# Kernel optimization log

Measured on AMD Instinct MI355X. Metric: run time of the kernel, lower is better.

Reference implementation:

```python
import jax, jax.numpy as jnp
import numpy as np

BETA = 0.95
THR = 0.8
SLOPE = 25.0  # fast_sigmoid surrogate slope


@jax.custom_vjp
def spike(x):
    # Heaviside forward, fast-sigmoid surrogate backward (snntorch surrogate.fast_sigmoid)
    return (x > 0).astype(x.dtype)

def _spike_fwd(x):
    return spike(x), x

def _spike_bwd(x, g):
    return (g / (SLOPE * jnp.abs(x) + 1.0) ** 2,)

spike.defvjp(_spike_fwd, _spike_bwd)


def setup_inputs() -> dict:
    key = jax.random.key(0)
    k1, k2, k3 = jax.random.split(key, 3)
    B, T, D, H, C = 512, 2000, 20, 128, 10
    x = jax.random.normal(k1, (B, T, D), dtype=jnp.float32)
    # kaiming_normal_ with nonlinearity='linear': std = 1/sqrt(fan_in)
    W1 = jax.random.normal(k2, (H, D), dtype=jnp.float32) / np.sqrt(D)
    b1 = jnp.zeros((H,), jnp.float32)
    W2 = jax.random.normal(k3, (C, H), dtype=jnp.float32) / np.sqrt(H)
    b2 = jnp.zeros((C,), jnp.float32)
    return {"x": x, "W1": W1, "b1": b1, "W2": W2, "b2": b2}


def reference(x, W1, b1, W2, b2):
    B, T, D = x.shape
    H = W1.shape[0]

    def step(mem, xt):
        cur = xt @ W1.T + b1                                  # [B,H]
        # snntorch Leaky: reset based on PREVIOUS mem (detached), subtract mechanism
        reset = jax.lax.stop_gradient(spike(mem - THR))
        mem_new = BETA * mem + cur - reset * THR
        spk = spike(mem_new - THR)
        return mem_new, spk

    mem0 = jnp.zeros((B, H), x.dtype)
    _, spks = jax.lax.scan(step, mem0, jnp.swapaxes(x, 0, 1))  # spks: [T,B,H]

    spikeCounts = spks.sum(0)                                  # [B,H]
    # sum_t fc2(spk_t) = spikeCounts @ W2^T + T * b2
    logits = (spikeCounts @ W2.T + T * b2) / T
    logits = logits + 0.1 * ((spikeCounts / (T + 1e-6)) @ W2.T + b2)
    return logits
```

## Files before the change

kernel.cpp:

```cpp
#include <hip/hip_runtime.h>
#include <stdint.h>

#define Bdim 512
#define Tdim 2000
#define Ddim 20
#define Hdim 128
#define Cdim 10
#define TT   64
#define NCH  32
#define BETA 0.95f
#define THR  0.8f

typedef float f32x2 __attribute__((ext_vector_type(2)));
typedef float f32x4 __attribute__((ext_vector_type(4)));
typedef int   i32x4 __attribute__((ext_vector_type(4)));

#define CVT_HILO(HI, LO, F0, F1) {                                                     \
    asm volatile("v_cvt_pk_bf16_f32 %0, %1, %2" : "=v"(HI) : "v"(F0), "v"(F1));        \
    const float h0f_ = __uint_as_float((HI) << 16);                                    \
    const float h1f_ = __uint_as_float((HI) & 0xFFFF0000u);                            \
    const float l0_ = (F0) - h0f_;  const float l1_ = (F1) - h1f_;                     \
    asm volatile("v_cvt_pk_bf16_f32 %0, %1, %2" : "=v"(LO) : "v"(l0_), "v"(l1_)); }

#define MFMA0(ACC, A8, B8) \
  asm volatile("v_mfma_f32_16x16x32_bf16 %0, %1, %2, 0"  : "=v"(ACC) : "v"(A8), "v"(B8));
#define MFMA(ACC, A8, B8)  \
  asm volatile("v_mfma_f32_16x16x32_bf16 %0, %1, %2, %0" : "+v"(ACC) : "v"(A8), "v"(B8));

__global__ __launch_bounds__(256, 1) void snn_spec4_kernel(
    const float* __restrict__ x,
    const float* __restrict__ W1,
    const float* __restrict__ b1,
    const float* __restrict__ W2,
    const float* __restrict__ b2,
    float* __restrict__ out)
{
  const int b   = blockIdx.x;
  const int tid = threadIdx.x;
  const int wid = tid >> 6;
  const int l   = tid & 63;
  const int r   = l & 15;
  const int g   = l >> 4;

  const bool flip = ((b >> 8) & 1) != 0;
  const bool isP  = flip ? (wid >= 2) : (wid < 2);
  const int  pwid = wid & 1;
  const int  swid = wid & 1;

  __shared__ __align__(16) float xraw[2][TT * Ddim];
  __shared__ __align__(16) float cur[2][TT * 132];
  __shared__ float cnt_s[Hdim];

  const float* xb = x + (size_t)b * (Tdim * Ddim);
  const float* const clampMax = x + (size_t)Bdim * Tdim * Ddim - 4;

  const uint32_t xrawB = (uint32_t)(uintptr_t)&xraw[0][0];
  const uint32_t curB  = (uint32_t)(uintptr_t)&cur[0][0];

  i32x4 bhi[8], blo[8];
  f32x4 zero4, ovr;
  bool  sel23 = false, g3f = false;
  if (isP) {
    const bool g2 = (g == 2);
    g3f   = (g == 3);
    sel23 = g2 | g3f;
    zero4[0]=0.f; zero4[1]=0.f; zero4[2]=0.f; zero4[3]=0.f;
    ovr = zero4; if (g2) ovr[0] = 1.0f;
#pragma unroll
    for (int ni = 0; ni < 8; ++ni) {
      const int hh = ni * 16 + r;
      float wv[8];
#pragma unroll
      for (int j = 0; j < 8; ++j) {
        const int k = 8 * g + j;
        wv[j] = (k < Ddim) ? W1[hh * Ddim + k] : ((k == Ddim) ? b1[hh] : 0.0f);
      }
#pragma unroll
      for (int d = 0; d < 4; ++d) {
        const uint32_t u0 = __float_as_uint(wv[2*d]), u1 = __float_as_uint(wv[2*d+1]);
        const uint32_t h0 = (u0 + 0x8000u) & 0xFFFF0000u;
        const uint32_t h1 = (u1 + 0x8000u) & 0xFFFF0000u;
        bhi[ni][d] = (int)(h1 | (h0 >> 16));
        const float l0 = wv[2*d]   - __uint_as_float(h0);
        const float l1 = wv[2*d+1] - __uint_as_float(h1);
        const uint32_t e0 = (__float_as_uint(l0) + 0x8000u) & 0xFFFF0000u;
        const uint32_t e1 = (__float_as_uint(l1) + 0x8000u) & 0xFFFF0000u;
        blo[ni][d] = (int)(e1 | (e0 >> 16));
      }
    }
  }

  float    mem = 0.0f;
  bool     sp  = false;
  uint32_t cnt = 0u;
  f32x2    negT2; negT2[0] = -THR; negT2[1] = -THR;

#define STAGE(CH, BUF) do {                                                            \
    const float* g0_ = xb + (CH) * 1280 + pwid * 640 + l * 4;                          \
    char* lb_ = (char*)&xraw[0][0] + (BUF) * 5120 + pwid * 2560 + l * 16;              \
    const float* p0_ = g0_;        if (p0_ > clampMax) p0_ = clampMax;                 \
    const float* p1_ = g0_ + 256;  if (p1_ > clampMax) p1_ = clampMax;                 \
    __builtin_amdgcn_global_load_lds(                                                  \
      (const __attribute__((address_space(1))) unsigned int*)p0_,                      \
      (__attribute__((address_space(3))) unsigned int*)lb_, 16, 0, 0);                 \
    __builtin_amdgcn_global_load_lds(                                                  \
      (const __attribute__((address_space(1))) unsigned int*)p1_,                      \
      (__attribute__((address_space(3))) unsigned int*)(lb_ + 1024), 16, 0, 0);        \
    if (l < 32) {                                                                      \
      const float* p2_ = g0_ + 512;  if (p2_ > clampMax) p2_ = clampMax;               \
      __builtin_amdgcn_global_load_lds(                                                \
        (const __attribute__((address_space(1))) unsigned int*)p2_,                    \
        (__attribute__((address_space(3))) unsigned int*)(lb_ + 2048), 16, 0, 0);      \
    } } while (0)

#define VM0()  asm volatile("s_waitcnt vmcnt(0)" ::: "memory");
#define LGW(N) asm volatile("s_waitcnt lgkmcnt(" #N ")" ::: "memory"); __builtin_amdgcn_sched_barrier(0);
#define BAR()  __builtin_amdgcn_sched_barrier(0); __builtin_amdgcn_s_barrier(); __builtin_amdgcn_sched_barrier(0);

#define CW2(NI, AC)                                                                    \
    asm volatile("ds_write2_b32 %0, %1, %2 offset0:%c3 offset1:%c4"                    \
                 :: "v"(cwb_),  "v"(AC[0]), "v"(AC[1]), "n"(16*(NI)), "n"(16*(NI)+132)); \
    asm volatile("ds_write2_b32 %0, %1, %2 offset0:%c3 offset1:%c4"                    \
                 :: "v"(cwb2_), "v"(AC[2]), "v"(AC[3]), "n"(16*(NI)), "n"(16*(NI)+132));

#define CWRM(MTIDX, P0,P1,P2,P3,P4,P5,P6,P7) {                                         \
    const uint32_t cwb_  = curB + (uint32_t)(pbuf * 33792 + 528 * ((MTIDX) * 16 + 4 * g) + 4 * r); \
    const uint32_t cwb2_ = cwb_ + 1056u;                                               \
    CW2(0,P0) CW2(1,P1) CW2(2,P2) CW2(3,P3) CW2(4,P4) CW2(5,P5) CW2(6,P6) CW2(7,P7) }

#define SELA(A0, A1) { A0 = g3f ? zero4 : A0;  A1 = sel23 ? ovr : A1; }

#define CVT8(AHI, ALO, A0, A1) {                                                       \
    uint32_t h_, lo_;                                                                  \
    CVT_HILO(h_, lo_, A0[0], A0[1]) AHI[0]=(int)h_; ALO[0]=(int)lo_;                   \
    CVT_HILO(h_, lo_, A0[2], A0[3]) AHI[1]=(int)h_; ALO[1]=(int)lo_;                   \
    CVT_HILO(h_, lo_, A1[0], A1[1]) AHI[2]=(int)h_; ALO[2]=(int)lo_;                   \
    CVT_HILO(h_, lo_, A1[2], A1[3]) AHI[3]=(int)h_; ALO[3]=(int)lo_; }

#define MM24(AHI, ALO, C0,C1,C2,C3,C4,C5,C6,C7)                                        \
    MFMA0(C0, ALO, bhi[0]) MFMA0(C1, ALO, bhi[1]) MFMA0(C2, ALO, bhi[2])               \
    MFMA0(C3, ALO, bhi[3]) MFMA0(C4, ALO, bhi[4]) MFMA0(C5, ALO, bhi[5])               \
    MFMA0(C6, ALO, bhi[6]) MFMA0(C7, ALO, bhi[7])                                      \
    MFMA (C0, AHI, blo[0]) MFMA (C1, AHI, blo[1]) MFMA (C2, AHI, blo[2])               \
    MFMA (C3, AHI, blo[3]) MFMA (C4, AHI, blo[4]) MFMA (C5, AHI, blo[5])               \
    MFMA (C6, AHI, blo[6]) MFMA (C7, AHI, blo[7])                                      \
    MFMA (C0, AHI, bhi[0]) MFMA (C1, AHI, bhi[1]) MFMA (C2, AHI, bhi[2])               \
    MFMA (C3, AHI, bhi[3]) MFMA (C4, AHI, bhi[4]) MFMA (C5, AHI, bhi[5])               \
    MFMA (C6, AHI, bhi[6]) MFMA (C7, AHI, bhi[7])

#define GEMM2() {                                                                      \
    const uint32_t afb_ = xrawB + (uint32_t)(pbuf * 5120 + (2*pwid) * 1280 + 80 * r + 32 * g); \
    f32x4 a00_, a01_, a10_, a11_;                                                      \
    asm volatile("ds_read_b128 %0, %1 offset:0"    : "=v"(a00_) : "v"(afb_));          \
    asm volatile("ds_read_b128 %0, %1 offset:16"   : "=v"(a01_) : "v"(afb_));          \
    asm volatile("ds_read_b128 %0, %1 offset:1280" : "=v"(a10_) : "v"(afb_));          \
    asm volatile("ds_read_b128 %0, %1 offset:1296" : "=v"(a11_) : "v"(afb_));          \
    LGW(2)                                                                             \
    SELA(a00_, a01_)                                                                   \
    i32x4 ahi0_, alo0_;  CVT8(ahi0_, alo0_, a00_, a01_)                                \
    asm volatile("s_nop 2");                                                           \
    f32x4 c00,c01,c02,c03,c04,c05,c06,c07;                                             \
    MM24(ahi0_, alo0_, c00,c01,c02,c03,c04,c05,c06,c07)                                \
    LGW(0)                                                                             \
    SELA(a10_, a11_)                                                                   \
    i32x4 ahi1_, alo1_;  CVT8(ahi1_, alo1_, a10_, a11_)                                \
    asm volatile("s_nop 2");                                                           \
    f32x4 c10,c11,c12,c13,c14,c15,c16,c17;                                             \
    MM24(ahi1_, alo1_, c10,c11,c12,c13,c14,c15,c16,c17)                                \
    asm volatile("s_nop 7"); asm volatile("s_nop 4");                                  \
    CWRM(2*pwid,     c00,c01,c02,c03,c04,c05,c06,c07)                                  \
    CWRM(2*pwid + 1, c10,c11,c12,c13,c14,c15,c16,c17) }

#define GEMM_TAIL() {                                                                  \
    const uint32_t afb_ = xrawB + (uint32_t)(pbuf * 5120 + 80 * r + 32 * g);           \
    f32x4 a00_, a01_;                                                                  \
    asm volatile("ds_read_b128 %0, %1 offset:0"  : "=v"(a00_) : "v"(afb_));            \
    asm volatile("ds_read_b128 %0, %1 offset:16" : "=v"(a01_) : "v"(afb_));            \
    LGW(0)                                                                             \
    SELA(a00_, a01_)                                                                   \
    i32x4 ahi0_, alo0_;  CVT8(ahi0_, alo0_, a00_, a01_)                                \
    asm volatile("s_nop 2");                                                           \
    f32x4 c00,c01,c02,c03,c04,c05,c06,c07;                                             \
    MM24(ahi0_, alo0_, c00,c01,c02,c03,c04,c05,c06,c07)                                \
    asm volatile("s_nop 7"); asm volatile("s_nop 4");                                  \
    CWRM(0, c00,c01,c02,c03,c04,c05,c06,c07) }

#define RD2A(PR, AD) asm volatile("ds_read2_b32 %0, %1 offset0:0 offset1:132" : "=v"(PR) : "v"(AD));
#define CONSUME(PR) {                                                                  \
    f32x2 cm_; asm("v_pk_add_f32 %0, %1, %2" : "=v"(cm_) : "v"(PR), "v"(negT2));       \
    float mP_ = fmaf(BETA, mem, PR[0]);                                                \
    float mM_ = fmaf(BETA, mem, cm_[0]);                                               \
    mem = sp ? mM_ : mP_;                                                              \
    sp  = mem > THR;                                                                   \
    cnt += sp ? 1u : 0u;                                                               \
    mP_ = fmaf(BETA, mem, PR[1]);                                                      \
    mM_ = fmaf(BETA, mem, cm_[1]);                                                     \
    mem = sp ? mM_ : mP_;                                                              \
    sp  = mem > THR;                                                                   \
    cnt += sp ? 1u : 0u; }

#define SFI(RGA, RGB, SA, SB) { LGW(6) CONSUME(pr##RGA) CONSUME(pr##RGB)               \
    { const uint32_t adA_ = spB + (uint32_t)((SA) * 1056); RD2A(pr##RGA, adA_) }       \
    { const uint32_t adB_ = spB + (uint32_t)((SB) * 1056); RD2A(pr##RGB, adB_) } }
#define SFT(RGA, RGB, W) { LGW(W) CONSUME(pr##RGA) CONSUME(pr##RGB) }

#define SCAN_PRE()                                                                     \
    f32x2 pr0, pr1, pr2, pr3, pr4, pr5, pr6, pr7;                                      \
    RD2A(pr0, spB)          RD2A(pr1, spB + 1056u)  RD2A(pr2, spB + 2112u)             \
    RD2A(pr3, spB + 3168u)  RD2A(pr4, spB + 4224u)  RD2A(pr5, spB + 5280u)             \
    RD2A(pr6, spB + 6336u)  RD2A(pr7, spB + 7392u)

#define SCAN_FULL() {                                                                  \
    SCAN_PRE()                                                                         \
    SFI(0,1,  8, 9) SFI(2,3, 10,11) SFI(4,5, 12,13) SFI(6,7, 14,15)                    \
    SFI(0,1, 16,17) SFI(2,3, 18,19) SFI(4,5, 20,21) SFI(6,7, 22,23)                    \
    SFI(0,1, 24,25) SFI(2,3, 26,27) SFI(4,5, 28,29) SFI(6,7, 30,31)                    \
    SFT(0,1,6) SFT(2,3,4) SFT(4,5,2) SFT(6,7,0) }

#define SCAN_TAIL() {                                                                  \
    SCAN_PRE()                                                                         \
    SFT(0,1,6) SFT(2,3,4) SFT(4,5,2) SFT(6,7,0) }

  const uint32_t spB0 = curB + (uint32_t)((swid * 64 + l) * 4);

  if (isP) STAGE(0, 0);

#pragma unroll 1
  for (int ph = 0; ph <= NCH; ++ph) {
    if (isP) {
      if (ph <= NCH - 1) {
        VM0()
        if (ph < NCH - 1) STAGE(ph + 1, (ph + 1) & 1);
        const uint32_t pbuf = (uint32_t)(ph & 1);
        if (ph < NCH - 1) {
          GEMM2()
        } else if (pwid == 0) {
          GEMM_TAIL()
        }
        LGW(0)
      }
    } else {
      if (ph >= 1) {
        const uint32_t spB = spB0 + (uint32_t)(((ph - 1) & 1) * 33792);
        if (ph - 1 < NCH - 1) { SCAN_FULL() }
        else                  { SCAN_TAIL() }
        if (ph == NCH) cnt_s[swid * 64 + l] = (float)cnt;
      }
    }
    BAR()
  }

  __syncthreads();

  if (tid < Cdim) {
    float dot = 0.0f;
#pragma unroll
    for (int k = 0; k < Hdim; ++k)
      dot = fmaf(cnt_s[k], W2[tid * Hdim + k], dot);
    const float Tf = (float)Tdim;
    const float scale = 1.0f / Tf + 0.1f / (Tf + 1e-6f);
    out[b * Cdim + tid] = fmaf(dot, scale, 1.1f * b2[tid]);
  }
}

extern "C" void kernel_launch(void* const* d_in, const int* in_sizes, int n_in,
                              void* d_out, int out_size, void* d_ws, size_t ws_size,
                              hipStream_t stream) {
  const float* x  = (const float*)d_in[0];
  const float* W1 = (const float*)d_in[1];
  const float* b1 = (const float*)d_in[2];
  const float* W2 = (const float*)d_in[3];
  const float* b2 = (const float*)d_in[4];
  float* out = (float*)d_out;

  snn_spec4_kernel<<<dim3(Bdim), dim3(256), 0, stream>>>(x, W1, b1, W2, b2, out);
}
```

Measured before the change: 58.73 us.

## Split hidden dimension across two blocks per batch row with atomic output reduction

Each batch row is now handled by two blocks, each owning half of the hidden units (64). The time chunk is halved to 32 steps so the GEMM and scan loops keep their shapes. Partial logits are combined with atomicAdd into an output zeroed by a memset beforehand. The aim is to double the grid to fill more CUs and shorten each block's serial scan work. The cost is that x is loaded twice, there are twice as many barrier phases, and an extra memset launch plus atomics are added.

```diff
diff --git a/kernel.cpp b/kernel.cpp
--- a/kernel.cpp
+++ b/kernel.cpp
@@ -6,8 +6,8 @@
 #define Ddim 20
 #define Hdim 128
 #define Cdim 10
-#define TT   64
-#define NCH  32
+#define TT   32
+#define NCHF 62
 #define BETA 0.95f
 #define THR  0.8f
 
@@ -27,7 +27,7 @@
 #define MFMA(ACC, A8, B8)  \
   asm volatile("v_mfma_f32_16x16x32_bf16 %0, %1, %2, %0" : "+v"(ACC) : "v"(A8), "v"(B8));
 
-__global__ __launch_bounds__(256, 1) void snn_spec4_kernel(
+__global__ __launch_bounds__(256, 1) void snn_spec5_kernel(
     const float* __restrict__ x,
     const float* __restrict__ W1,
     const float* __restrict__ b1,
@@ -35,29 +35,31 @@
     const float* __restrict__ b2,
     float* __restrict__ out)
 {
-  const int b   = blockIdx.x;
+  const int blk = blockIdx.x;
+  const int bb  = blk >> 1;
+  const int hh  = blk & 1;
   const int tid = threadIdx.x;
   const int wid = tid >> 6;
   const int l   = tid & 63;
   const int r   = l & 15;
   const int g   = l >> 4;
 
-  const bool flip = ((b >> 8) & 1) != 0;
+  const bool flip = ((blk >> 8) & 1) != 0;
   const bool isP  = flip ? (wid >= 2) : (wid < 2);
   const int  pwid = wid & 1;
   const int  swid = wid & 1;
 
   __shared__ __align__(16) float xraw[2][TT * Ddim];
-  __shared__ __align__(16) float cur[2][TT * 132];
-  __shared__ float cnt_s[Hdim];
-
-  const float* xb = x + (size_t)b * (Tdim * Ddim);
+  __shared__ __align__(16) float cur[2][TT * 66];
+  __shared__ float cnt_s[64];
+
+  const float* xb = x + (size_t)bb * (Tdim * Ddim);
   const float* const clampMax = x + (size_t)Bdim * Tdim * Ddim - 4;
 
   const uint32_t xrawB = (uint32_t)(uintptr_t)&xraw[0][0];
   const uint32_t curB  = (uint32_t)(uintptr_t)&cur[0][0];
 
-  i32x4 bhi[8], blo[8];
+  i32x4 bhi[4], blo[4];
   f32x4 zero4, ovr;
   bool  sel23 = false, g3f = false;
   if (isP) {
@@ -67,13 +69,13 @@
     zero4[0]=0.f; zero4[1]=0.f; zero4[2]=0.f; zero4[3]=0.f;
     ovr = zero4; if (g2) ovr[0] = 1.0f;
 #pragma unroll
-    for (int ni = 0; ni < 8; ++ni) {
-      const int hh = ni * 16 + r;
+    for (int ni = 0; ni < 4; ++ni) {
+      const int hhh = hh * 64 + ni * 16 + r;
       float wv[8];
 #pragma unroll
       for (int j = 0; j < 8; ++j) {
         const int k = 8 * g + j;
-        wv[j] = (k < Ddim) ? W1[hh * Ddim + k] : ((k == Ddim) ? b1[hh] : 0.0f);
+        wv[j] = (k < Ddim) ? W1[hhh * Ddim + k] : ((k == Ddim) ? b1[hhh] : 0.0f);
       }
 #pragma unroll
       for (int d = 0; d < 4; ++d) {
@@ -96,40 +98,24 @@
   f32x2    negT2; negT2[0] = -THR; negT2[1] = -THR;
 
 #define STAGE(CH, BUF) do {                                                            \
-    const float* g0_ = xb + (CH) * 1280 + pwid * 640 + l * 4;                          \
-    char* lb_ = (char*)&xraw[0][0] + (BUF) * 5120 + pwid * 2560 + l * 16;              \
-    const float* p0_ = g0_;        if (p0_ > clampMax) p0_ = clampMax;                 \
-    const float* p1_ = g0_ + 256;  if (p1_ > clampMax) p1_ = clampMax;                 \
+    const float* g0_ = xb + (CH) * 640 + pwid * 320 + l * 4;                           \
+    char* lb_ = (char*)&xraw[0][0] + (BUF) * 2560 + pwid * 1280 + l * 16;              \
+    const float* p0_ = g0_;  if (p0_ > clampMax) p0_ = clampMax;                       \
     __builtin_amdgcn_global_load_lds(                                                  \
       (const __attribute__((address_space(1))) unsigned int*)p0_,                      \
       (__attribute__((address_space(3))) unsigned int*)lb_, 16, 0, 0);                 \
-    __builtin_amdgcn_global_load_lds(                                                  \
-      (const __attribute__((address_space(1))) unsigned int*)p1_,                      \
-      (__attribute__((address_space(3))) unsigned int*)(lb_ + 1024), 16, 0, 0);        \
-    if (l < 32) {                                                                      \
-      const float* p2_ = g0_ + 512;  if (p2_ > clampMax) p2_ = clampMax;               \
+    if (l < 16) {                                                                      \
+      const float* p1_ = g0_ + 256;  if (p1_ > clampMax) p1_ = clampMax;               \
       __builtin_amdgcn_global_load_lds(                                                \
-        (const __attribute__((address_space(1))) unsigned int*)p2_,                    \
-        (__attribute__((address_space(3))) unsigned int*)(lb_ + 2048), 16, 0, 0);      \
+        (const __attribute__((address_space(1))) unsigned int*)p1_,                    \
+        (__attribute__((address_space(3))) unsigned int*)(lb_ + 1024), 16, 0, 0);      \
     } } while (0)
 
 #define VM0()  asm volatile("s_waitcnt vmcnt(0)" ::: "memory");
 #define LGW(N) asm volatile("s_waitcnt lgkmcnt(" #N ")" ::: "memory"); __builtin_amdgcn_sched_barrier(0);
 #define BAR()  __builtin_amdgcn_sched_barrier(0); __builtin_amdgcn_s_barrier(); __builtin_amdgcn_sched_barrier(0);
 
-#define CW2(NI, AC)                                                                    \
-    asm volatile("ds_write2_b32 %0, %1, %2 offset0:%c3 offset1:%c4"                    \
-                 :: "v"(cwb_),  "v"(AC[0]), "v"(AC[1]), "n"(16*(NI)), "n"(16*(NI)+132)); \
-    asm volatile("ds_write2_b32 %0, %1, %2 offset0:%c3 offset1:%c4"                    \
-                 :: "v"(cwb2_), "v"(AC[2]), "v"(AC[3]), "n"(16*(NI)), "n"(16*(NI)+132));
-
-#define CWRM(MTIDX, P0,P1,P2,P3,P4,P5,P6,P7) {                                         \
-    const uint32_t cwb_  = curB + (uint32_t)(pbuf * 33792 + 528 * ((MTIDX) * 16 + 4 * g) + 4 * r); \
-    const uint32_t cwb2_ = cwb_ + 1056u;                                               \
-    CW2(0,P0) CW2(1,P1) CW2(2,P2) CW2(3,P3) CW2(4,P4) CW2(5,P5) CW2(6,P6) CW2(7,P7) }
-
 #define SELA(A0, A1) { A0 = g3f ? zero4 : A0;  A1 = sel23 ? ovr : A1; }
-
 #define CVT8(AHI, ALO, A0, A1) {                                                       \
     uint32_t h_, lo_;                                                                  \
     CVT_HILO(h_, lo_, A0[0], A0[1]) AHI[0]=(int)h_; ALO[0]=(int)lo_;                   \
@@ -137,55 +123,37 @@
     CVT_HILO(h_, lo_, A1[0], A1[1]) AHI[2]=(int)h_; ALO[2]=(int)lo_;                   \
     CVT_HILO(h_, lo_, A1[2], A1[3]) AHI[3]=(int)h_; ALO[3]=(int)lo_; }
 
-#define MM24(AHI, ALO, C0,C1,C2,C3,C4,C5,C6,C7)                                        \
-    MFMA0(C0, ALO, bhi[0]) MFMA0(C1, ALO, bhi[1]) MFMA0(C2, ALO, bhi[2])               \
-    MFMA0(C3, ALO, bhi[3]) MFMA0(C4, ALO, bhi[4]) MFMA0(C5, ALO, bhi[5])               \
-    MFMA0(C6, ALO, bhi[6]) MFMA0(C7, ALO, bhi[7])                                      \
-    MFMA (C0, AHI, blo[0]) MFMA (C1, AHI, blo[1]) MFMA (C2, AHI, blo[2])               \
-    MFMA (C3, AHI, blo[3]) MFMA (C4, AHI, blo[4]) MFMA (C5, AHI, blo[5])               \
-    MFMA (C6, AHI, blo[6]) MFMA (C7, AHI, blo[7])                                      \
-    MFMA (C0, AHI, bhi[0]) MFMA (C1, AHI, bhi[1]) MFMA (C2, AHI, bhi[2])               \
-    MFMA (C3, AHI, bhi[3]) MFMA (C4, AHI, bhi[4]) MFMA (C5, AHI, bhi[5])               \
-    MFMA (C6, AHI, bhi[6]) MFMA (C7, AHI, bhi[7])
-
-#define GEMM2() {                                                                      \
-    const uint32_t afb_ = xrawB + (uint32_t)(pbuf * 5120 + (2*pwid) * 1280 + 80 * r + 32 * g); \
-    f32x4 a00_, a01_, a10_, a11_;                                                      \
-    asm volatile("ds_read_b128 %0, %1 offset:0"    : "=v"(a00_) : "v"(afb_));          \
-    asm volatile("ds_read_b128 %0, %1 offset:16"   : "=v"(a01_) : "v"(afb_));          \
-    asm volatile("ds_read_b128 %0, %1 offset:1280" : "=v"(a10_) : "v"(afb_));          \
-    asm volatile("ds_read_b128 %0, %1 offset:1296" : "=v"(a11_) : "v"(afb_));          \
-    LGW(2)                                                                             \
-    SELA(a00_, a01_)                                                                   \
-    i32x4 ahi0_, alo0_;  CVT8(ahi0_, alo0_, a00_, a01_)                                \
+#define MM12(AHI, ALO, C0,C1,C2,C3)                                                    \
+    MFMA0(C0, ALO, bhi[0]) MFMA0(C1, ALO, bhi[1])                                      \
+    MFMA0(C2, ALO, bhi[2]) MFMA0(C3, ALO, bhi[3])                                      \
+    MFMA (C0, AHI, blo[0]) MFMA (C1, AHI, blo[1])                                      \
+    MFMA (C2, AHI, blo[2]) MFMA (C3, AHI, blo[3])                                      \
+    MFMA (C0, AHI, bhi[0]) MFMA (C1, AHI, bhi[1])                                      \
+    MFMA (C2, AHI, bhi[2]) MFMA (C3, AHI, bhi[3])
+
+#define CW2(NI, AC)                                                                    \
+    asm volatile("ds_write2_b32 %0, %1, %2 offset0:%c3 offset1:%c4"                    \
+                 :: "v"(cwb_),  "v"(AC[0]), "v"(AC[1]), "n"(16*(NI)), "n"(16*(NI)+66)); \
+    asm volatile("ds_write2_b32 %0, %1, %2 offset0:%c3 offset1:%c4"                    \
+                 :: "v"(cwb2_), "v"(AC[2]), "v"(AC[3]), "n"(16*(NI)), "n"(16*(NI)+66));
+
+#define GEMM1(TLOC) {                                                                  \
+    const uint32_t afb_ = xrawB + (uint32_t)(pbuf * 2560 + (TLOC) * 80 + 80 * r + 32 * g); \
+    f32x4 a0_, a1_;                                                                    \
+    asm volatile("ds_read_b128 %0, %1 offset:0"  : "=v"(a0_) : "v"(afb_));             \
+    asm volatile("ds_read_b128 %0, %1 offset:16" : "=v"(a1_) : "v"(afb_));             \
+    LGW(0)                                                                             \
+    SELA(a0_, a1_)                                                                     \
+    i32x4 ahi_, alo_;  CVT8(ahi_, alo_, a0_, a1_)                                      \
     asm volatile("s_nop 2");                                                           \
-    f32x4 c00,c01,c02,c03,c04,c05,c06,c07;                                             \
-    MM24(ahi0_, alo0_, c00,c01,c02,c03,c04,c05,c06,c07)                                \
-    LGW(0)                                                                             \
-    SELA(a10_, a11_)                                                                   \
-    i32x4 ahi1_, alo1_;  CVT8(ahi1_, alo1_, a10_, a11_)                                \
-    asm volatile("s_nop 2");                                                           \
-    f32x4 c10,c11,c12,c13,c14,c15,c16,c17;                                             \
-    MM24(ahi1_, alo1_, c10,c11,c12,c13,c14,c15,c16,c17)                                \
+    f32x4 c0_, c1_, c2_, c3_;                                                          \
+    MM12(ahi_, alo_, c0_, c1_, c2_, c3_)                                               \
     asm volatile("s_nop 7"); asm volatile("s_nop 4");                                  \
-    CWRM(2*pwid,     c00,c01,c02,c03,c04,c05,c06,c07)                                  \
-    CWRM(2*pwid + 1, c10,c11,c12,c13,c14,c15,c16,c17) }
-
-#define GEMM_TAIL() {                                                                  \
-    const uint32_t afb_ = xrawB + (uint32_t)(pbuf * 5120 + 80 * r + 32 * g);           \
-    f32x4 a00_, a01_;                                                                  \
-    asm volatile("ds_read_b128 %0, %1 offset:0"  : "=v"(a00_) : "v"(afb_));            \
-    asm volatile("ds_read_b128 %0, %1 offset:16" : "=v"(a01_) : "v"(afb_));            \
-    LGW(0)                                                                             \
-    SELA(a00_, a01_)                                                                   \
-    i32x4 ahi0_, alo0_;  CVT8(ahi0_, alo0_, a00_, a01_)                                \
-    asm volatile("s_nop 2");                                                           \
-    f32x4 c00,c01,c02,c03,c04,c05,c06,c07;                                             \
-    MM24(ahi0_, alo0_, c00,c01,c02,c03,c04,c05,c06,c07)                                \
-    asm volatile("s_nop 7"); asm volatile("s_nop 4");                                  \
-    CWRM(0, c00,c01,c02,c03,c04,c05,c06,c07) }
-
-#define RD2A(PR, AD) asm volatile("ds_read2_b32 %0, %1 offset0:0 offset1:132" : "=v"(PR) : "v"(AD));
+    const uint32_t cwb_  = curB + (uint32_t)(pbuf * 8448 + 264 * ((TLOC) + 4 * g) + 4 * r); \
+    const uint32_t cwb2_ = cwb_ + 528u;                                                \
+    CW2(0, c0_) CW2(1, c1_) CW2(2, c2_) CW2(3, c3_) }
+
+#define RD2A(PR, AD) asm volatile("ds_read2_b32 %0, %1 offset0:0 offset1:66" : "=v"(PR) : "v"(AD));
 #define CONSUME(PR) {                                                                  \
     f32x2 cm_; asm("v_pk_add_f32 %0, %1, %2" : "=v"(cm_) : "v"(PR), "v"(negT2));       \
     float mP_ = fmaf(BETA, mem, PR[0]);                                                \
@@ -200,66 +168,65 @@
     cnt += sp ? 1u : 0u; }
 
 #define SFI(RGA, RGB, SA, SB) { LGW(6) CONSUME(pr##RGA) CONSUME(pr##RGB)               \
-    { const uint32_t adA_ = spB + (uint32_t)((SA) * 1056); RD2A(pr##RGA, adA_) }       \
-    { const uint32_t adB_ = spB + (uint32_t)((SB) * 1056); RD2A(pr##RGB, adB_) } }
+    { const uint32_t adA_ = spB + (uint32_t)((SA) * 528); RD2A(pr##RGA, adA_) }        \
+    { const uint32_t adB_ = spB + (uint32_t)((SB) * 528); RD2A(pr##RGB, adB_) } }
 #define SFT(RGA, RGB, W) { LGW(W) CONSUME(pr##RGA) CONSUME(pr##RGB) }
 
 #define SCAN_PRE()                                                                     \
     f32x2 pr0, pr1, pr2, pr3, pr4, pr5, pr6, pr7;                                      \
-    RD2A(pr0, spB)          RD2A(pr1, spB + 1056u)  RD2A(pr2, spB + 2112u)             \
-    RD2A(pr3, spB + 3168u)  RD2A(pr4, spB + 4224u)  RD2A(pr5, spB + 5280u)             \
-    RD2A(pr6, spB + 6336u)  RD2A(pr7, spB + 7392u)
-
-#define SCAN_FULL() {                                                                  \
+    RD2A(pr0, spB)          RD2A(pr1, spB + 528u)   RD2A(pr2, spB + 1056u)             \
+    RD2A(pr3, spB + 1584u)  RD2A(pr4, spB + 2112u)  RD2A(pr5, spB + 2640u)             \
+    RD2A(pr6, spB + 3168u)  RD2A(pr7, spB + 3696u)
+
+#define SCAN_FULL() {                                             \
     SCAN_PRE()                                                                         \
     SFI(0,1,  8, 9) SFI(2,3, 10,11) SFI(4,5, 12,13) SFI(6,7, 14,15)                    \
-    SFI(0,1, 16,17) SFI(2,3, 18,19) SFI(4,5, 20,21) SFI(6,7, 22,23)                    \
-    SFI(0,1, 24,25) SFI(2,3, 26,27) SFI(4,5, 28,29) SFI(6,7, 30,31)                    \
     SFT(0,1,6) SFT(2,3,4) SFT(4,5,2) SFT(6,7,0) }
 
-#define SCAN_TAIL() {                                                                  \
+#define SCAN_TAIL() {                                              \
     SCAN_PRE()                                                                         \
     SFT(0,1,6) SFT(2,3,4) SFT(4,5,2) SFT(6,7,0) }
 
-  const uint32_t spB0 = curB + (uint32_t)((swid * 64 + l) * 4);
+  const uint32_t spB0 = curB + (uint32_t)((swid * 32 + (l & 31)) * 4);
 
   if (isP) STAGE(0, 0);
 
 #pragma unroll 1
-  for (int ph = 0; ph <= NCH; ++ph) {
+  for (int ph = 0; ph <= NCHF + 1; ++ph) {
     if (isP) {
-      if (ph <= NCH - 1) {
+      if (ph <= NCHF) {
         VM0()
-        if (ph < NCH - 1) STAGE(ph + 1, (ph + 1) & 1);
+        if (ph < NCHF) STAGE(ph + 1, (ph + 1) & 1);
         const uint32_t pbuf = (uint32_t)(ph & 1);
-        if (ph < NCH - 1) {
-          GEMM2()
+        if (ph < NCHF) {
+          GEMM1(pwid * 16)
         } else if (pwid == 0) {
-          GEMM_TAIL()
+          GEMM1(0)
         }
         LGW(0)
       }
     } else {
       if (ph >= 1) {
-        const uint32_t spB = spB0 + (uint32_t)(((ph - 1) & 1) * 33792);
-        if (ph - 1 < NCH - 1) { SCAN_FULL() }
-        else                  { SCAN_TAIL() }
-        if (ph == NCH) cnt_s[swid * 64 + l] = (float)cnt;
+        const uint32_t spB = spB0 + (uint32_t)(((ph - 1) & 1) * 8448);
+        if (ph - 1 < NCHF) { SCAN_FULL() }
+        else               { SCAN_TAIL() }
       }
     }
     BAR()
   }
 
+  if (!isP && l < 32) cnt_s[swid * 32 + (l & 31)] = (float)cnt;
   __syncthreads();
 
   if (tid < Cdim) {
     float dot = 0.0f;
 #pragma unroll
-    for (int k = 0; k < Hdim; ++k)
-      dot = fmaf(cnt_s[k], W2[tid * Hdim + k], dot);
+    for (int k = 0; k < 64; ++k)
+      dot = fmaf(cnt_s[k], W2[tid * Hdim + hh * 64 + k], dot);
     const float Tf = (float)Tdim;
     const float scale = 1.0f / Tf + 0.1f / (Tf + 1e-6f);
-    out[b * Cdim + tid] = fmaf(dot, scale, 1.1f * b2[tid]);
+    float val = dot * scale + (hh == 0 ? 1.1f * b2[tid] : 0.0f);
+    atomicAdd(&out[bb * Cdim + tid], val);
   }
 }
 
@@ -273,5 +240,6 @@
   const float* b2 = (const float*)d_in[4];
   float* out = (float*)d_out;
 
-  snn_spec4_kernel<<<dim3(Bdim), dim3(256), 0, stream>>>(x, W1, b1, W2, b2, out);
+  hipMemsetAsync(out, 0, (size_t)Bdim * Cdim * sizeof(float), stream);
+  snn_spec5_kernel<<<dim3(Bdim * 2), dim3(256), 0, stream>>>(x, W1, b1, W2, b2, out);
 }
```

New measurement: 98.24 us. +67.3%, slower.

## Transpose cur staging buffer to hidden-major layout with 128-bit LDS writes/reads

Applied to the files above, without the earlier changes.

Changes the shared-memory cur buffer from time-major [T][132] to hidden-major [H][66] so each scan lane reads four consecutive timesteps with one ds_read_b128. The GEMM waves now store MFMA accumulator quads with ds_write_b128 instead of paired ds_write2_b32. This cuts the number of LDS instructions on both the producer and the consumer side of the serial scan. The padding of 66 floats per row is meant to avoid bank conflicts, but the wider accesses may still conflict.

```diff
diff --git a/kernel.cpp b/kernel.cpp
--- a/kernel.cpp
+++ b/kernel.cpp
@@ -27,7 +27,7 @@
 #define MFMA(ACC, A8, B8)  \
   asm volatile("v_mfma_f32_16x16x32_bf16 %0, %1, %2, %0" : "+v"(ACC) : "v"(A8), "v"(B8));
 
-__global__ __launch_bounds__(256, 1) void snn_spec4_kernel(
+__global__ __launch_bounds__(256, 1) void snn_spec6_kernel(
     const float* __restrict__ x,
     const float* __restrict__ W1,
     const float* __restrict__ b1,
@@ -48,7 +48,7 @@
   const int  swid = wid & 1;
 
   __shared__ __align__(16) float xraw[2][TT * Ddim];
-  __shared__ __align__(16) float cur[2][TT * 132];
+  __shared__ __align__(16) float cur[2][Hdim * 66];
   __shared__ float cnt_s[Hdim];
 
   const float* xb = x + (size_t)b * (Tdim * Ddim);
@@ -117,17 +117,6 @@
 #define LGW(N) asm volatile("s_waitcnt lgkmcnt(" #N ")" ::: "memory"); __builtin_amdgcn_sched_barrier(0);
 #define BAR()  __builtin_amdgcn_sched_barrier(0); __builtin_amdgcn_s_barrier(); __builtin_amdgcn_sched_barrier(0);
 
-#define CW2(NI, AC)                                                                    \
-    asm volatile("ds_write2_b32 %0, %1, %2 offset0:%c3 offset1:%c4"                    \
-                 :: "v"(cwb_),  "v"(AC[0]), "v"(AC[1]), "n"(16*(NI)), "n"(16*(NI)+132)); \
-    asm volatile("ds_write2_b32 %0, %1, %2 offset0:%c3 offset1:%c4"                    \
-                 :: "v"(cwb2_), "v"(AC[2]), "v"(AC[3]), "n"(16*(NI)), "n"(16*(NI)+132));
-
-#define CWRM(MTIDX, P0,P1,P2,P3,P4,P5,P6,P7) {                                         \
-    const uint32_t cwb_  = curB + (uint32_t)(pbuf * 33792 + 528 * ((MTIDX) * 16 + 4 * g) + 4 * r); \
-    const uint32_t cwb2_ = cwb_ + 1056u;                                               \
-    CW2(0,P0) CW2(1,P1) CW2(2,P2) CW2(3,P3) CW2(4,P4) CW2(5,P5) CW2(6,P6) CW2(7,P7) }
-
 #define SELA(A0, A1) { A0 = g3f ? zero4 : A0;  A1 = sel23 ? ovr : A1; }
 
 #define CVT8(AHI, ALO, A0, A1) {                                                       \
@@ -147,6 +136,12 @@
     MFMA (C0, AHI, bhi[0]) MFMA (C1, AHI, bhi[1]) MFMA (C2, AHI, bhi[2])               \
     MFMA (C3, AHI, bhi[3]) MFMA (C4, AHI, bhi[4]) MFMA (C5, AHI, bhi[5])               \
     MFMA (C6, AHI, bhi[6]) MFMA (C7, AHI, bhi[7])
+
+#define WQ(CWB, AC, NI) \
+    asm volatile("ds_write_b128 %0, %1 offset:%c2" :: "v"(CWB), "v"(AC), "n"(4224*(NI)));
+#define WTILE8(CWB, P0,P1,P2,P3,P4,P5,P6,P7)                                           \
+    WQ(CWB,P0,0) WQ(CWB,P1,1) WQ(CWB,P2,2) WQ(CWB,P3,3)                                \
+    WQ(CWB,P4,4) WQ(CWB,P5,5) WQ(CWB,P6,6) WQ(CWB,P7,7)
 
 #define GEMM2() {                                                                      \
     const uint32_t afb_ = xrawB + (uint32_t)(pbuf * 5120 + (2*pwid) * 1280 + 80 * r + 32 * g); \
@@ -168,8 +163,9 @@
     f32x4 c10,c11,c12,c13,c14,c15,c16,c17;                                             \
     MM24(ahi1_, alo1_, c10,c11,c12,c13,c14,c15,c16,c17)                                \
     asm volatile("s_nop 7"); asm volatile("s_nop 4");                                  \
-    CWRM(2*pwid,     c00,c01,c02,c03,c04,c05,c06,c07)                                  \
-    CWRM(2*pwid + 1, c10,c11,c12,c13,c14,c15,c16,c17) }
+    const uint32_t cwA_ = curB + (uint32_t)(pbuf * 33792 + 264 * r + 128 * pwid + 16 * g); \
+    WTILE8(cwA_,       c00,c01,c02,c03,c04,c05,c06,c07)                                \
+    WTILE8(cwA_ + 64u, c10,c11,c12,c13,c14,c15,c16,c17) }
 
 #define GEMM_TAIL() {                                                                  \
     const uint32_t afb_ = xrawB + (uint32_t)(pbuf * 5120 + 80 * r + 32 * g);           \
@@ -183,45 +179,73 @@
     f32x4 c00,c01,c02,c03,c04,c05,c06,c07;                                             \
     MM24(ahi0_, alo0_, c00,c01,c02,c03,c04,c05,c06,c07)                                \
     asm volatile("s_nop 7"); asm volatile("s_nop 4");                                  \
-    CWRM(0, c00,c01,c02,c03,c04,c05,c06,c07) }
-
-#define RD2A(PR, AD) asm volatile("ds_read2_b32 %0, %1 offset0:0 offset1:132" : "=v"(PR) : "v"(AD));
-#define CONSUME(PR) {                                                                  \
-    f32x2 cm_; asm("v_pk_add_f32 %0, %1, %2" : "=v"(cm_) : "v"(PR), "v"(negT2));       \
-    float mP_ = fmaf(BETA, mem, PR[0]);                                                \
-    float mM_ = fmaf(BETA, mem, cm_[0]);                                               \
+    const uint32_t cwT_ = curB + (uint32_t)(pbuf * 33792 + 264 * r + 16 * g);          \
+    WTILE8(cwT_, c00,c01,c02,c03,c04,c05,c06,c07) }
+
+#define RDQ(Q, AD, OFF) \
+    asm volatile("ds_read_b128 %0, %1 offset:%c2" : "=v"(Q) : "v"(AD), "n"(OFF));
+
+#define CONSUME2(C0V, C1V) {                                                           \
+    float mP_ = fmaf(BETA, mem, C0V);                                                  \
+    float mM_ = fmaf(BETA, mem, C0V - THR);                                            \
     mem = sp ? mM_ : mP_;                                                              \
     sp  = mem > THR;                                                                   \
     cnt += sp ? 1u : 0u;                                                               \
-    mP_ = fmaf(BETA, mem, PR[1]);                                                      \
-    mM_ = fmaf(BETA, mem, cm_[1]);                                                     \
+    mP_ = fmaf(BETA, mem, C1V);                                                        \
+    mM_ = fmaf(BETA, mem, C1V - THR);                                                  \
     mem = sp ? mM_ : mP_;                                                              \
     sp  = mem > THR;                                                                   \
     cnt += sp ? 1u : 0u; }
 
-#define SFI(RGA, RGB, SA, SB) { LGW(6) CONSUME(pr##RGA) CONSUME(pr##RGB)               \
-    { const uint32_t adA_ = spB + (uint32_t)((SA) * 1056); RD2A(pr##RGA, adA_) }       \
-    { const uint32_t adB_ = spB + (uint32_t)((SB) * 1056); RD2A(pr##RGB, adB_) } }
-#define SFT(RGA, RGB, W) { LGW(W) CONSUME(pr##RGA) CONSUME(pr##RGB) }
-
-#define SCAN_PRE()                                                                     \
-    f32x2 pr0, pr1, pr2, pr3, pr4, pr5, pr6, pr7;                                      \
-    RD2A(pr0, spB)          RD2A(pr1, spB + 1056u)  RD2A(pr2, spB + 2112u)             \
-    RD2A(pr3, spB + 3168u)  RD2A(pr4, spB + 4224u)  RD2A(pr5, spB + 5280u)             \
-    RD2A(pr6, spB + 6336u)  RD2A(pr7, spB + 7392u)
-
-#define SCAN_FULL() {                                                                  \
-    SCAN_PRE()                                                                         \
-    SFI(0,1,  8, 9) SFI(2,3, 10,11) SFI(4,5, 12,13) SFI(6,7, 14,15)                    \
-    SFI(0,1, 16,17) SFI(2,3, 18,19) SFI(4,5, 20,21) SFI(6,7, 22,23)                    \
-    SFI(0,1, 24,25) SFI(2,3, 26,27) SFI(4,5, 28,29) SFI(6,7, 30,31)                    \
-    SFT(0,1,6) SFT(2,3,4) SFT(4,5,2) SFT(6,7,0) }
-
-#define SCAN_TAIL() {                                                                  \
-    SCAN_PRE()                                                                         \
-    SFT(0,1,6) SFT(2,3,4) SFT(4,5,2) SFT(6,7,0) }
-
-  const uint32_t spB0 = curB + (uint32_t)((swid * 64 + l) * 4);
+#define CONSUME4(Q) {                                                                  \
+    f32x2 p01_; p01_[0] = Q[0]; p01_[1] = Q[1];                                        \
+    f32x2 p23_; p23_[0] = Q[2]; p23_[1] = Q[3];                                        \
+    f32x2 cm01_, cm23_;                                                                \
+    asm("v_pk_add_f32 %0, %1, %2" : "=v"(cm01_) : "v"(p01_), "v"(negT2));              \
+    asm("v_pk_add_f32 %0, %1, %2" : "=v"(cm23_) : "v"(p23_), "v"(negT2));              \
+    { float mP_ = fmaf(BETA, mem, Q[0]);                                               \
+      float mM_ = fmaf(BETA, mem, cm01_[0]);                                           \
+      mem = sp ? mM_ : mP_;  sp = mem > THR;  cnt += sp ? 1u : 0u;                     \
+      mP_ = fmaf(BETA, mem, Q[1]);                                                     \
+      mM_ = fmaf(BETA, mem, cm01_[1]);                                                 \
+      mem = sp ? mM_ : mP_;  sp = mem > THR;  cnt += sp ? 1u : 0u;                     \
+      mP_ = fmaf(BETA, mem, Q[2]);                                                     \
+      mM_ = fmaf(BETA, mem, cm23_[0]);                                                 \
+      mem = sp ? mM_ : mP_;  sp = mem > THR;  cnt += sp ? 1u : 0u;                     \
+      mP_ = fmaf(BETA, mem, Q[3]);                                                     \
+      mM_ = fmaf(BETA, mem, cm23_[1]);                                                 \
+      mem = sp ? mM_ : mP_;  sp = mem > THR;  cnt += sp ? 1u : 0u; } }
+
+#define SCAN_FULL(SPB) {                                                               \
+    f32x4 q0,q1,q2,q3,q4,q5;                                                           \
+    RDQ(q0,SPB,0)  RDQ(q1,SPB,16) RDQ(q2,SPB,32)                                       \
+    RDQ(q3,SPB,48) RDQ(q4,SPB,64) RDQ(q5,SPB,80)                                       \
+    LGW(5) CONSUME4(q0) RDQ(q0,SPB,96)                                                 \
+    LGW(5) CONSUME4(q1) RDQ(q1,SPB,112)                                                \
+    LGW(5) CONSUME4(q2) RDQ(q2,SPB,128)                                                \
+    LGW(5) CONSUME4(q3) RDQ(q3,SPB,144)                                                \
+    LGW(5) CONSUME4(q4) RDQ(q4,SPB,160)                                                \
+    LGW(5) CONSUME4(q5) RDQ(q5,SPB,176)                                                \
+    LGW(5) CONSUME4(q0) RDQ(q0,SPB,192)                                                \
+    LGW(5) CONSUME4(q1) RDQ(q1,SPB,208)                                                \
+    LGW(5) CONSUME4(q2) RDQ(q2,SPB,224)                                                \
+    LGW(5) CONSUME4(q3) RDQ(q3,SPB,240)                                                \
+    LGW(5) CONSUME4(q4)                                                                \
+    LGW(4) CONSUME4(q5)                                                                \
+    LGW(3) CONSUME4(q0)                                                                \
+    LGW(2) CONSUME4(q1)                                                                \
+    LGW(1) CONSUME4(q2)                                                                \
+    LGW(0) CONSUME4(q3) }
+
+#define SCAN_TAIL(SPB) {                                                               \
+    f32x4 q0,q1,q2,q3;                                                                 \
+    RDQ(q0,SPB,0) RDQ(q1,SPB,16) RDQ(q2,SPB,32) RDQ(q3,SPB,48)                         \
+    LGW(3) CONSUME4(q0)                                                                \
+    LGW(2) CONSUME4(q1)                                                                \
+    LGW(1) CONSUME4(q2)                                                                \
+    LGW(0) CONSUME4(q3) }
+
+  const uint32_t spB0 = curB + (uint32_t)((swid * 64 + l) * 264);
 
   if (isP) STAGE(0, 0);
 
@@ -242,8 +266,8 @@
     } else {
       if (ph >= 1) {
         const uint32_t spB = spB0 + (uint32_t)(((ph - 1) & 1) * 33792);
-        if (ph - 1 < NCH - 1) { SCAN_FULL() }
-        else                  { SCAN_TAIL() }
+        if (ph - 1 < NCH - 1) { SCAN_FULL(spB) }
+        else                  { SCAN_TAIL(spB) }
         if (ph == NCH) cnt_s[swid * 64 + l] = (float)cnt;
       }
     }
@@ -273,5 +297,5 @@
   const float* b2 = (const float*)d_in[4];
   float* out = (float*)d_out;
 
-  snn_spec4_kernel<<<dim3(Bdim), dim3(256), 0, stream>>>(x, W1, b1, W2, b2, out);
+  snn_spec6_kernel<<<dim3(Bdim), dim3(256), 0, stream>>>(x, W1, b1, W2, b2, out);
 }
```

Result: slower. 122.9 us (+109.3%).

## Double waves per block: four GEMM producer and four scan consumer waves

Applied to the files above, without the earlier changes.

Block size grows from 256 to 512 threads. Each producer wave now handles one 16-row time tile instead of two, and each scan wave covers 32 hidden units instead of 64, with the upper 32 lanes duplicating the work. Staging loads are split over four waves, and the per-block flip of the producer/consumer role assignment is removed. The goal is to shorten the per-chunk critical path of both the GEMM and the serial scan, at the cost of more waves per block, redundant scan lanes and more barrier participants.

```diff
diff --git a/kernel.cpp b/kernel.cpp
--- a/kernel.cpp
+++ b/kernel.cpp
@@ -27,7 +27,7 @@
 #define MFMA(ACC, A8, B8)  \
   asm volatile("v_mfma_f32_16x16x32_bf16 %0, %1, %2, %0" : "+v"(ACC) : "v"(A8), "v"(B8));
 
-__global__ __launch_bounds__(256, 1) void snn_spec4_kernel(
+__global__ __launch_bounds__(512, 1) void snn_spec8_kernel(
     const float* __restrict__ x,
     const float* __restrict__ W1,
     const float* __restrict__ b1,
@@ -42,10 +42,9 @@
   const int r   = l & 15;
   const int g   = l >> 4;
 
-  const bool flip = ((b >> 8) & 1) != 0;
-  const bool isP  = flip ? (wid >= 2) : (wid < 2);
-  const int  pwid = wid & 1;
-  const int  swid = wid & 1;
+  const bool isP  = (wid < 4);
+  const int  pwid = wid & 3;
+  const int  swid = wid & 3;
 
   __shared__ __align__(16) float xraw[2][TT * Ddim];
   __shared__ __align__(16) float cur[2][TT * 132];
@@ -96,21 +95,17 @@
   f32x2    negT2; negT2[0] = -THR; negT2[1] = -THR;
 
 #define STAGE(CH, BUF) do {                                                            \
-    const float* g0_ = xb + (CH) * 1280 + pwid * 640 + l * 4;                          \
-    char* lb_ = (char*)&xraw[0][0] + (BUF) * 5120 + pwid * 2560 + l * 16;              \
-    const float* p0_ = g0_;        if (p0_ > clampMax) p0_ = clampMax;                 \
-    const float* p1_ = g0_ + 256;  if (p1_ > clampMax) p1_ = clampMax;                 \
+    const float* g0_ = xb + (CH) * 1280 + pwid * 320 + l * 4;                          \
+    char* lb_ = (char*)&xraw[0][0] + (BUF) * 5120 + pwid * 1280 + l * 16;              \
+    const float* p0_ = g0_;  if (p0_ > clampMax) p0_ = clampMax;                       \
     __builtin_amdgcn_global_load_lds(                                                  \
       (const __attribute__((address_space(1))) unsigned int*)p0_,                      \
       (__attribute__((address_space(3))) unsigned int*)lb_, 16, 0, 0);                 \
-    __builtin_amdgcn_global_load_lds(                                                  \
-      (const __attribute__((address_space(1))) unsigned int*)p1_,                      \
-      (__attribute__((address_space(3))) unsigned int*)(lb_ + 1024), 16, 0, 0);        \
-    if (l < 32) {                                                                      \
-      const float* p2_ = g0_ + 512;  if (p2_ > clampMax) p2_ = clampMax;               \
+    if (l < 16) {                                                                      \
+      const float* p1_ = g0_ + 256;  if (p1_ > clampMax) p1_ = clampMax;               \
       __builtin_amdgcn_global_load_lds(                                                \
-        (const __attribute__((address_space(1))) unsigned int*)p2_,                    \
-        (__attribute__((address_space(3))) unsigned int*)(lb_ + 2048), 16, 0, 0);      \
+        (const __attribute__((address_space(1))) unsigned int*)p1_,                    \
+        (__attribute__((address_space(3))) unsigned int*)(lb_ + 1024), 16, 0, 0);      \
     } } while (0)
 
 #define VM0()  asm volatile("s_waitcnt vmcnt(0)" ::: "memory");
@@ -148,31 +143,8 @@
     MFMA (C3, AHI, bhi[3]) MFMA (C4, AHI, bhi[4]) MFMA (C5, AHI, bhi[5])               \
     MFMA (C6, AHI, bhi[6]) MFMA (C7, AHI, bhi[7])
 
-#define GEMM2() {                                                                      \
-    const uint32_t afb_ = xrawB + (uint32_t)(pbuf * 5120 + (2*pwid) * 1280 + 80 * r + 32 * g); \
-    f32x4 a00_, a01_, a10_, a11_;                                                      \
-    asm volatile("ds_read_b128 %0, %1 offset:0"    : "=v"(a00_) : "v"(afb_));          \
-    asm volatile("ds_read_b128 %0, %1 offset:16"   : "=v"(a01_) : "v"(afb_));          \
-    asm volatile("ds_read_b128 %0, %1 offset:1280" : "=v"(a10_) : "v"(afb_));          \
-    asm volatile("ds_read_b128 %0, %1 offset:1296" : "=v"(a11_) : "v"(afb_));          \
-    LGW(2)                                                                             \
-    SELA(a00_, a01_)                                                                   \
-    i32x4 ahi0_, alo0_;  CVT8(ahi0_, alo0_, a00_, a01_)                                \
-    asm volatile("s_nop 2");                                                           \
-    f32x4 c00,c01,c02,c03,c04,c05,c06,c07;                                             \
-    MM24(ahi0_, alo0_, c00,c01,c02,c03,c04,c05,c06,c07)                                \
-    LGW(0)                                                                             \
-    SELA(a10_, a11_)                                                                   \
-    i32x4 ahi1_, alo1_;  CVT8(ahi1_, alo1_, a10_, a11_)                                \
-    asm volatile("s_nop 2");                                                           \
-    f32x4 c10,c11,c12,c13,c14,c15,c16,c17;                                             \
-    MM24(ahi1_, alo1_, c10,c11,c12,c13,c14,c15,c16,c17)                                \
-    asm volatile("s_nop 7"); asm volatile("s_nop 4");                                  \
-    CWRM(2*pwid,     c00,c01,c02,c03,c04,c05,c06,c07)                                  \
-    CWRM(2*pwid + 1, c10,c11,c12,c13,c14,c15,c16,c17) }
-
-#define GEMM_TAIL() {                                                                  \
-    const uint32_t afb_ = xrawB + (uint32_t)(pbuf * 5120 + 80 * r + 32 * g);           \
+#define GEMM1() {                                                                      \
+    const uint32_t afb_ = xrawB + (uint32_t)(pbuf * 5120 + pwid * 1280 + 80 * r + 32 * g); \
     f32x4 a00_, a01_;                                                                  \
     asm volatile("ds_read_b128 %0, %1 offset:0"  : "=v"(a00_) : "v"(afb_));            \
     asm volatile("ds_read_b128 %0, %1 offset:16" : "=v"(a01_) : "v"(afb_));            \
@@ -183,7 +155,7 @@
     f32x4 c00,c01,c02,c03,c04,c05,c06,c07;                                             \
     MM24(ahi0_, alo0_, c00,c01,c02,c03,c04,c05,c06,c07)                                \
     asm volatile("s_nop 7"); asm volatile("s_nop 4");                                  \
-    CWRM(0, c00,c01,c02,c03,c04,c05,c06,c07) }
+    CWRM(pwid, c00,c01,c02,c03,c04,c05,c06,c07) }
 
 #define RD2A(PR, AD) asm volatile("ds_read2_b32 %0, %1 offset0:0 offset1:132" : "=v"(PR) : "v"(AD));
 #define CONSUME(PR) {                                                                  \
@@ -221,7 +193,7 @@
     SCAN_PRE()                                                                         \
     SFT(0,1,6) SFT(2,3,4) SFT(4,5,2) SFT(6,7,0) }
 
-  const uint32_t spB0 = curB + (uint32_t)((swid * 64 + l) * 4);
+  const uint32_t spB0 = curB + (uint32_t)((swid * 32 + (l & 31)) * 4);
 
   if (isP) STAGE(0, 0);
 
@@ -233,9 +205,9 @@
         if (ph < NCH - 1) STAGE(ph + 1, (ph + 1) & 1);
         const uint32_t pbuf = (uint32_t)(ph & 1);
         if (ph < NCH - 1) {
-          GEMM2()
+          GEMM1()
         } else if (pwid == 0) {
-          GEMM_TAIL()
+          GEMM1()
         }
         LGW(0)
       }
@@ -244,7 +216,7 @@
         const uint32_t spB = spB0 + (uint32_t)(((ph - 1) & 1) * 33792);
         if (ph - 1 < NCH - 1) { SCAN_FULL() }
         else                  { SCAN_TAIL() }
-        if (ph == NCH) cnt_s[swid * 64 + l] = (float)cnt;
+        if (ph == NCH && l < 32) cnt_s[swid * 32 + (l & 31)] = (float)cnt;
       }
     }
     BAR()
@@ -273,5 +245,5 @@
   const float* b2 = (const float*)d_in[4];
   float* out = (float*)d_out;
 
-  snn_spec4_kernel<<<dim3(Bdim), dim3(256), 0, stream>>>(x, W1, b1, W2, b2, out);
+  snn_spec8_kernel<<<dim3(Bdim), dim3(512), 0, stream>>>(x, W1, b1, W2, b2, out);
 }
```

Measured after the change: 79.53 us. 35.4% more time.
